# Kernel tuning notes

Hardware: AMD Instinct MI355X
Metric: run time of the kernel (lower is better)

Reference implementation:

```python
import jax, jax.numpy as jnp
import numpy as np

NUM_USERS = 100000
NUM_ITEMS = 100000
D = 64          # embed_dim
B = 4096        # batch of users (rows of sparse interaction matrix)
NNZ = 204800    # nonzeros in sparse user-item matrix (~50 items/user)
N = 1048576     # number of (user,item) pairs to score
DROPOUT = 0.2


def setup_inputs() -> dict:
    key = jax.random.key(0)
    ks = jax.random.split(key, 10)
    return {
        "user_ids": jax.random.randint(ks[0], (B,), 0, NUM_USERS, dtype=jnp.int32),
        "bat_idx": jax.random.randint(ks[1], (N,), 0, B, dtype=jnp.int32),
        "sp_row": jax.random.randint(ks[2], (NNZ,), 0, B, dtype=jnp.int32),
        "sp_col": jax.random.randint(ks[3], (NNZ,), 0, NUM_ITEMS, dtype=jnp.int32),
        "bat_items": jax.random.randint(ks[4], (N,), 0, NUM_ITEMS, dtype=jnp.int32),
        # learned parameters (normal init for embeddings, zeros for offset/bias, as in reset_parameters)
        "en_emb": jax.random.normal(ks[5], (NUM_ITEMS, D), dtype=jnp.float32) * 0.01,
        "en_offset": jnp.zeros((D,), dtype=jnp.float32),
        "de_emb": jax.random.normal(ks[6], (NUM_ITEMS, D), dtype=jnp.float32) * 0.01,
        "de_bias": jnp.zeros((NUM_ITEMS,), dtype=jnp.float32),
        "user_emb": jax.random.normal(ks[7], (NUM_USERS, D), dtype=jnp.float32) * 0.01,
    }


def reference(user_ids, bat_idx, sp_row, sp_col, bat_items,
              en_emb, en_offset, de_emb, de_bias, user_emb):
    keep = 1.0 - DROPOUT
    # dropout_sparse: bernoulli keep-mask on sparse nnz values (binary 1.0), rescaled by 1/keep
    drop_mask = jax.random.bernoulli(jax.random.key(42), keep, (NNZ,))
    vals = drop_mask.astype(en_emb.dtype) / keep  # corrupted sparse values [NNZ]

    # sparse @ dense: sum_j A[b,j] * en_emb[j]  ->  gather + segment_sum  -> [B, D]
    hidden = jax.ops.segment_sum(vals[:, None] * en_emb[sp_col], sp_row, num_segments=B)
    hidden = jnp.tanh(hidden + user_emb[user_ids] + en_offset[None, :])

    # decode: inner product of gathered hidden rows and item embeddings
    h = hidden[bat_idx]                      # [N, D]
    de_i = de_emb[bat_items]                 # [N, D]
    ratings = jnp.sum(h * de_i, axis=-1) + de_bias[bat_items]  # [N]

    # l2 reg over unique bat_items rows (mask-based == torch.unique gather)
    item_mask = jnp.zeros((NUM_ITEMS,), en_emb.dtype).at[bat_items].set(1.0)
    reg_loss = 0.5 * (
        jnp.sum(item_mask * jnp.sum(en_emb ** 2, axis=-1))
        + jnp.sum(en_offset ** 2)
        + jnp.sum(user_emb[user_ids] ** 2)
        + jnp.sum(item_mask * jnp.sum(de_emb ** 2, axis=-1))
        + jnp.sum(item_mask * de_bias ** 2)
    )
    return ratings, reg_loss
```

## Files before the change

kernel.cpp:

```cpp
#include <hip/hip_runtime.h>
#include <hip/hip_bf16.h>

#define PARTITIONABLE 1
#define NB 8
#define CAPB 136192
#define FATB 2048
#define CAPR 128
#define RSB 200
#define HBLK 1024
#define REGB 1024

__device__ __forceinline__ unsigned rotl32(unsigned x, int r) {
    return (x << r) | (x >> (32 - r));
}

__device__ __forceinline__ void threefry2x32(unsigned k0, unsigned k1,
                                             unsigned& x0, unsigned& x1) {
    unsigned ks0 = k0, ks1 = k1, ks2 = k0 ^ k1 ^ 0x1BD11BDAu;
    x0 += ks0; x1 += ks1;
#define TF_R(r) { x0 += x1; x1 = rotl32(x1, r); x1 ^= x0; }
    TF_R(13) TF_R(15) TF_R(26) TF_R(6)   x0 += ks1; x1 += ks2 + 1u;
    TF_R(17) TF_R(29) TF_R(16) TF_R(24)  x0 += ks2; x1 += ks0 + 2u;
    TF_R(13) TF_R(15) TF_R(26) TF_R(6)   x0 += ks0; x1 += ks1 + 3u;
    TF_R(17) TF_R(29) TF_R(16) TF_R(24)  x0 += ks1; x1 += ks2 + 4u;
    TF_R(13) TF_R(15) TF_R(26) TF_R(6)   x0 += ks2; x1 += ks0 + 5u;
#undef TF_R
}

__device__ __forceinline__ bool keep_mask(int i, int nnz) {
#if PARTITIONABLE
    unsigned x0 = 0u, x1 = (unsigned)i;
    threefry2x32(0u, 42u, x0, x1);
    unsigned bits = x0 ^ x1;
#else
    int half = nnz >> 1;
    int j = (i < half) ? i : i - half;
    unsigned x0 = (unsigned)j, x1 = (unsigned)(j + half);
    threefry2x32(0u, 42u, x0, x1);
    unsigned bits = (i < half) ? x0 : x1;
#endif
    float u = __uint_as_float((bits >> 9) | 0x3f800000u) - 1.0f;
    return u < 0.8f;
}

__device__ __forceinline__ unsigned short f2bf(float f) {
    unsigned u = __float_as_uint(f);
    return (unsigned short)((u + 0x7FFFu + ((u >> 16) & 1u)) >> 16);
}

__device__ __forceinline__ float bfdot8(uint4 h, uint4 d) {
    float s;
    s  = __uint_as_float(h.x << 16)         * __uint_as_float(d.x << 16);
    s += __uint_as_float(h.x & 0xFFFF0000u) * __uint_as_float(d.x & 0xFFFF0000u);
    s += __uint_as_float(h.y << 16)         * __uint_as_float(d.y << 16);
    s += __uint_as_float(h.y & 0xFFFF0000u) * __uint_as_float(d.y & 0xFFFF0000u);
    s += __uint_as_float(h.z << 16)         * __uint_as_float(d.z << 16);
    s += __uint_as_float(h.z & 0xFFFF0000u) * __uint_as_float(d.z & 0xFFFF0000u);
    s += __uint_as_float(h.w << 16)         * __uint_as_float(d.w << 16);
    s += __uint_as_float(h.w & 0xFFFF0000u) * __uint_as_float(d.w & 0xFFFF0000u);
    return s;
}

__global__ void k_prep(const int* __restrict__ bat_idx, const int* __restrict__ bat_items,
                       unsigned char* __restrict__ mask, int* __restrict__ cursor,
                       unsigned* __restrict__ perm, unsigned* __restrict__ inv,
                       const int* __restrict__ sp_row, const int* __restrict__ sp_col,
                       int* __restrict__ rowcur, unsigned* __restrict__ srow,
                       int N, int num_items, int nnz, int B) {
    __shared__ int sh[4096];
    if (blockIdx.x < 256) {
        if (threadIdx.x < NB) sh[threadIdx.x] = 0;
        __syncthreads();
        const int per = N / 256;
        const int base_n = blockIdx.x * per;
        const int iters = per / blockDim.x;
        unsigned packed[16];
        int bkt[16];
        for (int it = 0; it < iters; ++it) {
            int n = base_n + it * blockDim.x + threadIdx.x;
            int item = bat_items[n];
            int bidx = bat_idx[n];
            mask[item] = 1;
            int b = (int)(((unsigned long long)(unsigned)item * NB) / (unsigned)num_items);
            packed[it] = ((unsigned)item << 12) | (unsigned)bidx;
            bkt[it] = b;
            atomicAdd(&sh[b], 1);
        }
        __syncthreads();
        if (threadIdx.x < NB) {
            int c = sh[threadIdx.x];
            sh[threadIdx.x] = atomicAdd(&cursor[threadIdx.x], c);
        }
        __syncthreads();
        for (int it = 0; it < iters; ++it) {
            int n = base_n + it * blockDim.x + threadIdx.x;
            int pos = atomicAdd(&sh[bkt[it]], 1);
            unsigned gpos = (unsigned)bkt[it] * CAPB + (unsigned)min(pos, CAPB - 1);
            perm[gpos] = packed[it];
            inv[n] = gpos;
        }
    } else {
        const int blk = blockIdx.x - 256;
        for (int i = threadIdx.x; i < B; i += blockDim.x) sh[i] = 0;
        __syncthreads();
        const int per = nnz / RSB;
        const int base = blk * per;
        const int iters = per / blockDim.x;
        unsigned pk[8];
        int rw[8];
        for (int it = 0; it < iters; ++it) {
            int i = base + it * blockDim.x + threadIdx.x;
            int row = sp_row[i];
            int col = sp_col[i];
            bool k = keep_mask(i, nnz);
            pk[it] = (unsigned)col;
            rw[it] = k ? row : -1;
            if (k) atomicAdd(&sh[row], 1);
        }
        __syncthreads();
        for (int i = threadIdx.x; i < B; i += blockDim.x) {
            int c = sh[i];
            if (c) sh[i] = atomicAdd(&rowcur[i], c);
        }
        __syncthreads();
        for (int it = 0; it < iters; ++it) {
            if (rw[it] >= 0) {
                int pos = atomicAdd(&sh[rw[it]], 1);
                srow[(size_t)rw[it] * CAPR + min(pos, CAPR - 1)] = pk[it];
            }
        }
    }
}

__global__ void k_hidden_reg(const unsigned* __restrict__ srow, const int* __restrict__ rowcur,
                             const float* __restrict__ en_emb, const float* __restrict__ user_emb,
                             const int* __restrict__ user_ids, const float* __restrict__ en_off,
                             unsigned short* __restrict__ hb,
                             const unsigned char* __restrict__ mask,
                             const float* __restrict__ de_emb, const float* __restrict__ de_bias,
                             unsigned short* __restrict__ debf,
                             float* __restrict__ reg_ws, int B, int num_items) {
    if (blockIdx.x < HBLK) {
        const int lane = threadIdx.x & 63;
        const int row = (blockIdx.x * blockDim.x + threadIdx.x) >> 6;
        if (row >= B) return;
        const int cnt = min(rowcur[row], CAPR);
        const unsigned* sr = srow + (size_t)row * CAPR;
        float acc0 = 0.f, acc1 = 0.f, acc2 = 0.f, acc3 = 0.f;
        float acc4 = 0.f, acc5 = 0.f, acc6 = 0.f, acc7 = 0.f;
        for (int j0 = 0; j0 < cnt; j0 += 64) {
            unsigned ev = (j0 + lane < cnt) ? sr[j0 + lane] : 0u;
            int m = min(64, cnt - j0);
            int jj = 0;
            for (; jj + 7 < m; jj += 8) {
                unsigned e0 = __shfl(ev, jj);
                unsigned e1 = __shfl(ev, jj + 1);
                unsigned e2 = __shfl(ev, jj + 2);
                unsigned e3 = __shfl(ev, jj + 3);
                unsigned e4 = __shfl(ev, jj + 4);
                unsigned e5 = __shfl(ev, jj + 5);
                unsigned e6 = __shfl(ev, jj + 6);
                unsigned e7 = __shfl(ev, jj + 7);
                acc0 += en_emb[(size_t)e0 * 64 + lane];
                acc1 += en_emb[(size_t)e1 * 64 + lane];
                acc2 += en_emb[(size_t)e2 * 64 + lane];
                acc3 += en_emb[(size_t)e3 * 64 + lane];
                acc4 += en_emb[(size_t)e4 * 64 + lane];
                acc5 += en_emb[(size_t)e5 * 64 + lane];
                acc6 += en_emb[(size_t)e6 * 64 + lane];
                acc7 += en_emb[(size_t)e7 * 64 + lane];
            }
            for (; jj + 3 < m; jj += 4) {
                unsigned e0 = __shfl(ev, jj);
                unsigned e1 = __shfl(ev, jj + 1);
                unsigned e2 = __shfl(ev, jj + 2);
                unsigned e3 = __shfl(ev, jj + 3);
                acc0 += en_emb[(size_t)e0 * 64 + lane];
                acc1 += en_emb[(size_t)e1 * 64 + lane];
                acc2 += en_emb[(size_t)e2 * 64 + lane];
                acc3 += en_emb[(size_t)e3 * 64 + lane];
            }
            for (; jj < m; ++jj) {
                unsigned e0 = __shfl(ev, jj);
                acc0 += en_emb[(size_t)e0 * 64 + lane];
            }
        }
        int uid = user_ids[row];
        float hval = 1.25f * (((acc0 + acc1) + (acc2 + acc3))
                            + ((acc4 + acc5) + (acc6 + acc7)))
                   + user_emb[(size_t)uid * 64 + lane] + en_off[lane];
        hb[(size_t)row * 64 + lane] = f2bf(tanhf(hval));
    } else {
        const int bx = blockIdx.x - HBLK;
        const int stride = REGB * blockDim.x;
        float s = 0.f;
        for (int t = bx * blockDim.x + threadIdx.x; t < num_items * 16; t += stride) {
            int i = t >> 4, l = t & 15;
            float4 d = *reinterpret_cast<const float4*>(de_emb + (size_t)i * 64 + l * 4);
            float4 e = *reinterpret_cast<const float4*>(en_emb + (size_t)i * 64 + l * 4);
            float m = (float)mask[i];
            ushort4 o;
            o.x = f2bf(d.x); o.y = f2bf(d.y); o.z = f2bf(d.z); o.w = f2bf(d.w);
            reinterpret_cast<ushort4*>(debf)[t] = o;
            float q = e.x*e.x + e.y*e.y + e.z*e.z + e.w*e.w
                    + d.x*d.x + d.y*d.y + d.z*d.z + d.w*d.w;
            if (l == 0) { float bb = de_bias[i]; q += bb * bb; }
            s += m * q;
        }
        for (int t = bx * blockDim.x + threadIdx.x; t < B * 16; t += stride) {
            int b = t >> 4, l = t & 15;
            int uid = user_ids[b];
            float4 u = *reinterpret_cast<const float4*>(user_emb + (size_t)uid * 64 + l * 4);
            s += u.x*u.x + u.y*u.y + u.z*u.z + u.w*u.w;
        }
        if (bx == 0 && threadIdx.x < 64) {
            float o = en_off[threadIdx.x];
            s += o * o;
        }
        for (int m = 1; m < 64; m <<= 1) s += __shfl_xor(s, m);
        __shared__ float wsum[4];
        if ((threadIdx.x & 63) == 0) wsum[threadIdx.x >> 6] = s;
        __syncthreads();
        if (threadIdx.x == 0)
            atomicAdd(reg_ws, wsum[0] + wsum[1] + wsum[2] + wsum[3]);
    }
}

__global__ void k_ratings_bkt(const unsigned short* __restrict__ hb,
                              const unsigned short* __restrict__ debf,
                              const float* __restrict__ de_bias,
                              const unsigned* __restrict__ perm, const int* __restrict__ cursor,
                              float* __restrict__ r_perm) {
    const int bkt = blockIdx.x & (NB - 1);
    const int cnt = cursor[bkt];
    const int l = threadIdx.x & 7;
    const int gid = (blockIdx.x >> 3) * (blockDim.x >> 3) + (threadIdx.x >> 3);
    const int gpb = (gridDim.x >> 3) * (blockDim.x >> 3);
    const unsigned* pb = perm + (size_t)bkt * CAPB;
    float* rb = r_perm + (size_t)bkt * CAPB;

    int slot = gid;
    for (; slot + 3 * gpb < cnt; slot += 4 * gpb) {
        unsigned p0 = pb[slot];
        unsigned p1 = pb[slot + gpb];
        unsigned p2 = pb[slot + 2 * gpb];
        unsigned p3 = pb[slot + 3 * gpb];
        int it0 = (int)(p0 >> 12), b0 = (int)(p0 & 0xFFFu);
        int it1 = (int)(p1 >> 12), b1 = (int)(p1 & 0xFFFu);
        int it2 = (int)(p2 >> 12), b2 = (int)(p2 & 0xFFFu);
        int it3 = (int)(p3 >> 12), b3 = (int)(p3 & 0xFFFu);
        uint4 h0 = *reinterpret_cast<const uint4*>(hb   + (size_t)b0  * 64 + l * 8);
        uint4 d0 = *reinterpret_cast<const uint4*>(debf + (size_t)it0 * 64 + l * 8);
        uint4 h1 = *reinterpret_cast<const uint4*>(hb   + (size_t)b1  * 64 + l * 8);
        uint4 d1 = *reinterpret_cast<const uint4*>(debf + (size_t)it1 * 64 + l * 8);
        uint4 h2 = *reinterpret_cast<const uint4*>(hb   + (size_t)b2  * 64 + l * 8);
        uint4 d2 = *reinterpret_cast<const uint4*>(debf + (size_t)it2 * 64 + l * 8);
        uint4 h3 = *reinterpret_cast<const uint4*>(hb   + (size_t)b3  * 64 + l * 8);
        uint4 d3 = *reinterpret_cast<const uint4*>(debf + (size_t)it3 * 64 + l * 8);
        float s0 = bfdot8(h0, d0);
        float s1 = bfdot8(h1, d1);
        float s2 = bfdot8(h2, d2);
        float s3 = bfdot8(h3, d3);
        s0 += __shfl_xor(s0, 1); s1 += __shfl_xor(s1, 1);
        s2 += __shfl_xor(s2, 1); s3 += __shfl_xor(s3, 1);
        s0 += __shfl_xor(s0, 2); s1 += __shfl_xor(s1, 2);
        s2 += __shfl_xor(s2, 2); s3 += __shfl_xor(s3, 2);
        s0 += __shfl_xor(s0, 4); s1 += __shfl_xor(s1, 4);
        s2 += __shfl_xor(s2, 4); s3 += __shfl_xor(s3, 4);
        if (l == 0) {
            rb[slot]           = s0 + de_bias[it0];
            rb[slot + gpb]     = s1 + de_bias[it1];
            rb[slot + 2 * gpb] = s2 + de_bias[it2];
            rb[slot + 3 * gpb] = s3 + de_bias[it3];
        }
    }
    for (; slot < cnt; slot += gpb) {
        unsigned p = pb[slot];
        int item = (int)(p >> 12), bidx = (int)(p & 0xFFFu);
        uint4 hv = *reinterpret_cast<const uint4*>(hb   + (size_t)bidx * 64 + l * 8);
        uint4 dv = *reinterpret_cast<const uint4*>(debf + (size_t)item * 64 + l * 8);
        float s = bfdot8(hv, dv);
        s += __shfl_xor(s, 1);
        s += __shfl_xor(s, 2);
        s += __shfl_xor(s, 4);
        if (l == 0) rb[slot] = s + de_bias[item];
    }
}

__global__ void k_unperm(const unsigned* __restrict__ inv, const float* __restrict__ r_perm,
                         const float* __restrict__ reg_ws, float* __restrict__ out, int N) {
    const int quads = N >> 2;
    const int stride = gridDim.x * blockDim.x;
    for (int q = blockIdx.x * blockDim.x + threadIdx.x; q < quads; q += stride) {
        uint4 iv = reinterpret_cast<const uint4*>(inv)[q];
        float4 o;
        o.x = r_perm[iv.x];
        o.y = r_perm[iv.y];
        o.z = r_perm[iv.z];
        o.w = r_perm[iv.w];
        reinterpret_cast<float4*>(out)[q] = o;
    }
    if (blockIdx.x == 0 && threadIdx.x == 0)
        out[N] = 0.5f * reg_ws[0];
}

__global__ void k_mask(const int* __restrict__ bat_items, unsigned char* __restrict__ mask,
                       int N) {
    int t = blockIdx.x * blockDim.x + threadIdx.x;
    if (t < N) mask[bat_items[t]] = 1;
}

__global__ void k_ratings(const float* __restrict__ hidden, const float* __restrict__ de_emb,
                          const float* __restrict__ de_bias,
                          const int* __restrict__ bat_idx, const int* __restrict__ bat_items,
                          float* __restrict__ out, int N) {
    const int l = threadIdx.x & 15;
    const int gid = (blockIdx.x * blockDim.x + threadIdx.x) >> 4;
    const int gstride = (gridDim.x * blockDim.x) >> 4;
    for (int n = gid; n < N; n += gstride) {
        int b  = bat_idx[n];
        int it = bat_items[n];
        float4 hv = *reinterpret_cast<const float4*>(hidden + (size_t)b  * 64 + l * 4);
        float4 dv = *reinterpret_cast<const float4*>(de_emb + (size_t)it * 64 + l * 4);
        float s = hv.x*dv.x + hv.y*dv.y + hv.z*dv.z + hv.w*dv.w;
        s += __shfl_xor(s, 1);
        s += __shfl_xor(s, 2);
        s += __shfl_xor(s, 4);
        s += __shfl_xor(s, 8);
        if (l == 0) out[n] = s + de_bias[it];
    }
}

__global__ void k_scatter(const int* __restrict__ sp_row, const int* __restrict__ sp_col,
                          const float* __restrict__ en_emb, float* __restrict__ hidden,
                          int nnz) {
    const int lane = threadIdx.x & 63;
    const int wave = (blockIdx.x * blockDim.x + threadIdx.x) >> 6;
    const int nwaves = (gridDim.x * blockDim.x) >> 6;
    for (int i = wave; i < nnz; i += nwaves) {
        if (!keep_mask(i, nnz)) continue;
        int row = sp_row[i];
        int col = sp_col[i];
        float v = 1.25f * en_emb[(size_t)col * 64 + lane];
        atomicAdd(&hidden[row * 64 + lane], v);
    }
}

__global__ void k_hfinish(float* __restrict__ hidden, const float* __restrict__ user_emb,
                          const int* __restrict__ user_ids, const float* __restrict__ en_off,
                          int B) {
    int t = blockIdx.x * blockDim.x + threadIdx.x;
    if (t >= B * 64) return;
    int b = t >> 6, d = t & 63;
    int uid = user_ids[b];
    float h = hidden[t] + user_emb[(size_t)uid * 64 + d] + en_off[d];
    hidden[t] = tanhf(h);
}

__global__ void k_reg_fb(const unsigned char* __restrict__ mask,
                         const float* __restrict__ en_emb, const float* __restrict__ de_emb,
                         const float* __restrict__ de_bias,
                         const float* __restrict__ user_emb, const int* __restrict__ user_ids,
                         const float* __restrict__ en_off,
                         float* __restrict__ reg, int num_items, int B) {
    const int stride = gridDim.x * blockDim.x;
    float s = 0.f;
    for (int t = blockIdx.x * blockDim.x + threadIdx.x; t < num_items * 16; t += stride) {
        int i = t >> 4, l = t & 15;
        if (mask[i]) {
            float4 e = *reinterpret_cast<const float4*>(en_emb + (size_t)i * 64 + l * 4);
            float4 d = *reinterpret_cast<const float4*>(de_emb + (size_t)i * 64 + l * 4);
            s += e.x*e.x + e.y*e.y + e.z*e.z + e.w*e.w
               + d.x*d.x + d.y*d.y + d.z*d.z + d.w*d.w;
            if (l == 0) { float bb = de_bias[i]; s += bb * bb; }
        }
    }
    for (int t = blockIdx.x * blockDim.x + threadIdx.x; t < B * 16; t += stride) {
        int b = t >> 4, l = t & 15;
        int uid = user_ids[b];
        float4 u = *reinterpret_cast<const float4*>(user_emb + (size_t)uid * 64 + l * 4);
        s += u.x*u.x + u.y*u.y + u.z*u.z + u.w*u.w;
    }
    if (blockIdx.x == 0 && threadIdx.x < 64) {
        float o = en_off[threadIdx.x];
        s += o * o;
    }
    for (int m = 1; m < 64; m <<= 1) s += __shfl_xor(s, m);
    __shared__ float wsum[4];
    if ((threadIdx.x & 63) == 0) wsum[threadIdx.x >> 6] = s;
    __syncthreads();
    if (threadIdx.x == 0)
        atomicAdd(reg, 0.5f * (wsum[0] + wsum[1] + wsum[2] + wsum[3]));
}

extern "C" void kernel_launch(void* const* d_in, const int* in_sizes, int n_in,
                              void* d_out, int out_size, void* d_ws, size_t ws_size,
                              hipStream_t stream) {
    const int*   user_ids  = (const int*)  d_in[0];
    const int*   bat_idx   = (const int*)  d_in[1];
    const int*   sp_row    = (const int*)  d_in[2];
    const int*   sp_col    = (const int*)  d_in[3];
    const int*   bat_items = (const int*)  d_in[4];
    const float* en_emb    = (const float*)d_in[5];
    const float* en_off    = (const float*)d_in[6];
    const float* de_emb    = (const float*)d_in[7];
    const float* de_bias   = (const float*)d_in[8];
    const float* user_emb  = (const float*)d_in[9];

    const int B         = in_sizes[0];
    const int N         = in_sizes[1];
    const int NNZ       = in_sizes[2];
    const int NUM_ITEMS = in_sizes[8];

    float* out = (float*)d_out;

    char* ws = (char*)d_ws;
    size_t off = 0;
    unsigned char* mask = (unsigned char*)(ws + off);
    off += ((size_t)NUM_ITEMS + 255) & ~(size_t)255;
    int* cursor = (int*)(ws + off);               off += 256;
    int* rowcur = (int*)(ws + off);               off += (size_t)B * 4;
    float* reg_ws = (float*)(ws + off);           off += 256;
    const size_t zero_bytes = off;
    float* hidden = (float*)(ws + off);           off += (size_t)B * 64 * 4;
    unsigned* perm   = (unsigned*)(ws + off);     off += (size_t)NB * CAPB * 4;
    unsigned* inv    = (unsigned*)(ws + off);     off += (size_t)N * 4;
    float*    r_perm = (float*)(ws + off);
    unsigned* srow   = (unsigned*)r_perm;
    size_t tail = (size_t)NB * CAPB * 4;
    if ((size_t)B * CAPR * 4 > tail) tail = (size_t)B * CAPR * 4;
    off += tail;
    unsigned short* hb   = (unsigned short*)(ws + off);  off += (size_t)B * 64 * 2;
    off = (off + 15) & ~(size_t)15;
    unsigned short* debf = (unsigned short*)(ws + off);  off += (size_t)NUM_ITEMS * 64 * 2;

    const bool sorted_path =
        (ws_size >= off) && (N == (1 << 20)) && (B == 4096) &&
        (NUM_ITEMS <= (1 << 17)) && (NUM_ITEMS >= 65536) &&
        (NUM_ITEMS % 4 == 0) &&
        (NNZ % (RSB * 256) == 0) && (NNZ / RSB <= CAPR * 256);

    hipMemsetAsync(ws, 0, zero_bytes, stream);

    if (sorted_path) {
        k_prep<<<256 + RSB, 256, 0, stream>>>(
            bat_idx, bat_items, mask, cursor, perm, inv,
            sp_row, sp_col, rowcur, srow, N, NUM_ITEMS, NNZ, B);
        k_hidden_reg<<<HBLK + REGB, 256, 0, stream>>>(
            srow, rowcur, en_emb, user_emb, user_ids, en_off, hb,
            mask, de_emb, de_bias, debf, reg_ws, B, NUM_ITEMS);
        k_ratings_bkt<<<FATB, 256, 0, stream>>>(hb, debf, de_bias, perm, cursor, r_perm);
        k_unperm<<<1024, 256, 0, stream>>>(inv, r_perm, reg_ws, out, N);
    } else {
        hipMemsetAsync(hidden, 0, (size_t)B * 64 * 4, stream);
        hipMemsetAsync(out + N, 0, sizeof(float), stream);
        k_mask<<<(N + 255) / 256, 256, 0, stream>>>(bat_items, mask, N);
        k_scatter<<<FATB, 256, 0, stream>>>(sp_row, sp_col, en_emb, hidden, NNZ);
        k_hfinish<<<(B * 64 + 255) / 256, 256, 0, stream>>>(hidden, user_emb, user_ids,
                                                            en_off, B);
        k_ratings<<<FATB, 256, 0, stream>>>(hidden, de_emb, de_bias, bat_idx, bat_items, out, N);
        k_reg_fb<<<REGB, 256, 0, stream>>>(mask, en_emb, de_emb, de_bias,
                                           user_emb, user_ids, en_off, out + N, NUM_ITEMS, B);
    }
}
```

Before: 180.6 us.

## Move bf16 conversion and per-item squared norms into the prep kernel

The de_emb bf16 conversion, per-item squared-norm computation and user/offset reg terms move out of the hidden/reg kernel into extra blocks of the prep kernel. There they run concurrently with the bucketing and sparse-row sort, since they do not depend on the mask. The hidden kernel's reg blocks now only do a masked sum over a precomputed per-item sq array. This costs an extra NUM_ITEMS float buffer and a larger prep launch. The fallback path's reg block count also changes.

```diff
diff --git a/kernel.cpp b/kernel.cpp
--- a/kernel.cpp
+++ b/kernel.cpp
@@ -7,8 +7,10 @@
 #define FATB 2048
 #define CAPR 128
 #define RSB 200
+#define SCVT 1024
 #define HBLK 1024
-#define REGB 1024
+#define REGF 64
+#define REGB_FB 256
 
 __device__ __forceinline__ unsigned rotl32(unsigned x, int r) {
     return (x << r) | (x >> (32 - r));
@@ -66,6 +68,11 @@
                        unsigned* __restrict__ perm, unsigned* __restrict__ inv,
                        const int* __restrict__ sp_row, const int* __restrict__ sp_col,
                        int* __restrict__ rowcur, unsigned* __restrict__ srow,
+                       const float* __restrict__ en_emb, const float* __restrict__ de_emb,
+                       const float* __restrict__ de_bias, const float* __restrict__ user_emb,
+                       const int* __restrict__ user_ids, const float* __restrict__ en_off,
+                       unsigned short* __restrict__ debf, float* __restrict__ sq,
+                       float* __restrict__ reg_ws,
                        int N, int num_items, int nnz, int B) {
     __shared__ int sh[4096];
     if (blockIdx.x < 256) {
@@ -99,7 +106,7 @@
             perm[gpos] = packed[it];
             inv[n] = gpos;
         }
-    } else {
+    } else if (blockIdx.x < 256 + RSB) {
         const int blk = blockIdx.x - 256;
         for (int i = threadIdx.x; i < B; i += blockDim.x) sh[i] = 0;
         __syncthreads();
@@ -129,6 +136,42 @@
                 srow[(size_t)rw[it] * CAPR + min(pos, CAPR - 1)] = pk[it];
             }
         }
+    } else {
+        const int bx = blockIdx.x - (256 + RSB);
+        const int stride = SCVT * blockDim.x;
+        for (int t = bx * blockDim.x + threadIdx.x; t < num_items * 16; t += stride) {
+            int i = t >> 4, l = t & 15;
+            float4 d = *reinterpret_cast<const float4*>(de_emb + (size_t)i * 64 + l * 4);
+            float4 e = *reinterpret_cast<const float4*>(en_emb + (size_t)i * 64 + l * 4);
+            ushort4 o;
+            o.x = f2bf(d.x); o.y = f2bf(d.y); o.z = f2bf(d.z); o.w = f2bf(d.w);
+            reinterpret_cast<ushort4*>(debf)[t] = o;
+            float q = e.x*e.x + e.y*e.y + e.z*e.z + e.w*e.w
+                    + d.x*d.x + d.y*d.y + d.z*d.z + d.w*d.w;
+            if (l == 0) { float bb = de_bias[i]; q += bb * bb; }
+            q += __shfl_xor(q, 1);
+            q += __shfl_xor(q, 2);
+            q += __shfl_xor(q, 4);
+            q += __shfl_xor(q, 8);
+            if (l == 0) sq[i] = q;
+        }
+        float s = 0.f;
+        for (int t = bx * blockDim.x + threadIdx.x; t < B * 16; t += stride) {
+            int b = t >> 4, l = t & 15;
+            int uid = user_ids[b];
+            float4 u = *reinterpret_cast<const float4*>(user_emb + (size_t)uid * 64 + l * 4);
+            s += u.x*u.x + u.y*u.y + u.z*u.z + u.w*u.w;
+        }
+        if (bx == 0 && threadIdx.x < 64) {
+            float o = en_off[threadIdx.x];
+            s += o * o;
+        }
+        for (int m = 1; m < 64; m <<= 1) s += __shfl_xor(s, m);
+        float* wsum = (float*)sh;
+        if ((threadIdx.x & 63) == 0) wsum[threadIdx.x >> 6] = s;
+        __syncthreads();
+        if (threadIdx.x == 0)
+            atomicAdd(reg_ws, wsum[0] + wsum[1] + wsum[2] + wsum[3]);
     }
 }
 
@@ -137,8 +180,7 @@
                              const int* __restrict__ user_ids, const float* __restrict__ en_off,
                              unsigned short* __restrict__ hb,
                              const unsigned char* __restrict__ mask,
-                             const float* __restrict__ de_emb, const float* __restrict__ de_bias,
-                             unsigned short* __restrict__ debf,
+                             const float* __restrict__ sq,
                              float* __restrict__ reg_ws, int B, int num_items) {
     if (blockIdx.x < HBLK) {
         const int lane = threadIdx.x & 63;
@@ -192,31 +234,10 @@
         hb[(size_t)row * 64 + lane] = f2bf(tanhf(hval));
     } else {
         const int bx = blockIdx.x - HBLK;
-        const int stride = REGB * blockDim.x;
+        const int stride = REGF * blockDim.x;
         float s = 0.f;
-        for (int t = bx * blockDim.x + threadIdx.x; t < num_items * 16; t += stride) {
-            int i = t >> 4, l = t & 15;
-            float4 d = *reinterpret_cast<const float4*>(de_emb + (size_t)i * 64 + l * 4);
-            float4 e = *reinterpret_cast<const float4*>(en_emb + (size_t)i * 64 + l * 4);
-            float m = (float)mask[i];
-            ushort4 o;
-            o.x = f2bf(d.x); o.y = f2bf(d.y); o.z = f2bf(d.z); o.w = f2bf(d.w);
-            reinterpret_cast<ushort4*>(debf)[t] = o;
-            float q = e.x*e.x + e.y*e.y + e.z*e.z + e.w*e.w
-                    + d.x*d.x + d.y*d.y + d.z*d.z + d.w*d.w;
-            if (l == 0) { float bb = de_bias[i]; q += bb * bb; }
-            s += m * q;
-        }
-        for (int t = bx * blockDim.x + threadIdx.x; t < B * 16; t += stride) {
-            int b = t >> 4, l = t & 15;
-            int uid = user_ids[b];
-            float4 u = *reinterpret_cast<const float4*>(user_emb + (size_t)uid * 64 + l * 4);
-            s += u.x*u.x + u.y*u.y + u.z*u.z + u.w*u.w;
-        }
-        if (bx == 0 && threadIdx.x < 64) {
-            float o = en_off[threadIdx.x];
-            s += o * o;
-        }
+        for (int i = bx * blockDim.x + threadIdx.x; i < num_items; i += stride)
+            s += (float)mask[i] * sq[i];
         for (int m = 1; m < 64; m <<= 1) s += __shfl_xor(s, m);
         __shared__ float wsum[4];
         if ((threadIdx.x & 63) == 0) wsum[threadIdx.x >> 6] = s;
@@ -433,6 +454,7 @@
     unsigned short* hb   = (unsigned short*)(ws + off);  off += (size_t)B * 64 * 2;
     off = (off + 15) & ~(size_t)15;
     unsigned short* debf = (unsigned short*)(ws + off);  off += (size_t)NUM_ITEMS * 64 * 2;
+    float* sq = (float*)(ws + off);                      off += (size_t)NUM_ITEMS * 4;
 
     const bool sorted_path =
         (ws_size >= off) && (N == (1 << 20)) && (B == 4096) &&
@@ -443,12 +465,14 @@
     hipMemsetAsync(ws, 0, zero_bytes, stream);
 
     if (sorted_path) {
-        k_prep<<<256 + RSB, 256, 0, stream>>>(
+        k_prep<<<256 + RSB + SCVT, 256, 0, stream>>>(
             bat_idx, bat_items, mask, cursor, perm, inv,
-            sp_row, sp_col, rowcur, srow, N, NUM_ITEMS, NNZ, B);
-        k_hidden_reg<<<HBLK + REGB, 256, 0, stream>>>(
+            sp_row, sp_col, rowcur, srow,
+            en_emb, de_emb, de_bias, user_emb, user_ids, en_off,
+            debf, sq, reg_ws, N, NUM_ITEMS, NNZ, B);
+        k_hidden_reg<<<HBLK + REGF, 256, 0, stream>>>(
             srow, rowcur, en_emb, user_emb, user_ids, en_off, hb,
-            mask, de_emb, de_bias, debf, reg_ws, B, NUM_ITEMS);
+            mask, sq, reg_ws, B, NUM_ITEMS);
         k_ratings_bkt<<<FATB, 256, 0, stream>>>(hb, debf, de_bias, perm, cursor, r_perm);
         k_unperm<<<1024, 256, 0, stream>>>(inv, r_perm, reg_ws, out, N);
     } else {
@@ -459,7 +483,7 @@
         k_hfinish<<<(B * 64 + 255) / 256, 256, 0, stream>>>(hidden, user_emb, user_ids,
                                                             en_off, B);
         k_ratings<<<FATB, 256, 0, stream>>>(hidden, de_emb, de_bias, bat_idx, bat_items, out, N);
-        k_reg_fb<<<REGB, 256, 0, stream>>>(mask, en_emb, de_emb, de_bias,
-                                           user_emb, user_ids, en_off, out + N, NUM_ITEMS, B);
-    }
-}
+        k_reg_fb<<<REGB_FB, 256, 0, stream>>>(mask, en_emb, de_emb, de_bias,
+                                              user_emb, user_ids, en_off, out + N, NUM_ITEMS, B);
+    }
+}
```

Result: no change. 178.8 us (-1.0%).
